# Optimization experiments

Measured on AMD Instinct MI355X. Metric: run time of the kernel, lower is better.

Reference implementation:

```python
import jax, jax.numpy as jnp
import numpy as np

N_LEVELS = 7  # log2(64) + 1

def setup_inputs() -> dict:
    key = jax.random.key(0)
    k1, k2, k3 = jax.random.split(key, 3)
    B, C, H, W = 32, 3, 64, 64
    flat_dim = C  # patch_size = 1
    n_embd = 896
    inner = n_embd // N_LEVELS  # 128
    return {
        "x": jax.random.normal(k1, (B, C, H, W), dtype=jnp.float32),
        "emb_w": jax.random.normal(k2, (flat_dim * N_LEVELS, n_embd), dtype=jnp.float32) * 0.05,
        "emb_b": jnp.zeros((n_embd,), dtype=jnp.float32),
        "cls_w": jax.random.normal(k3, (inner, 1000), dtype=jnp.float32) * 0.05,
        "cls_b": jnp.zeros((1000,), dtype=jnp.float32),
    }

def _token_tree(xp):
    # xp: (B, H, W, fd). For level l, every token gets the mean of its
    # aligned 2^l x 2^l block (quad-tree pooling), broadcast back to HxW.
    B, H, W, fd = xp.shape
    levels = []
    for l in range(N_LEVELS):
        bs = 2 ** l
        m = xp.reshape(B, H // bs, bs, W // bs, bs, fd).mean(axis=(2, 4))
        m = jnp.repeat(jnp.repeat(m, bs, axis=1), bs, axis=2)
        levels.append(m)
    return jnp.stack(levels, axis=3)  # (B, H, W, L, fd)

def reference(x, emb_w, emb_b, cls_w, cls_b):
    B, C, H, W = x.shape
    # patch extraction with patch_size=1 -> (B, H, W, C)
    xp = jnp.transpose(x, (0, 2, 3, 1))
    tree = _token_tree(xp)                      # (B,H,W,L,fd)
    flat = tree.reshape(B, H, W, -1)            # (B,H,W,L*fd)
    emb = flat @ emb_w + emb_b                  # (B,H,W,n_embd)
    inner = emb.shape[-1] // N_LEVELS
    emb = emb.reshape(B, H, W, N_LEVELS, inner)
    # num_layers = 0 -> nn.Sequential() is identity
    root = emb[:, :, :, N_LEVELS - 1, :]        # (B,H,W,inner)
    root_avg = root.mean(axis=(1, 2))           # (B,inner)
    return root_avg @ cls_w + cls_b             # (B,1000)
```

## Files before the change

kernel.cpp:

```cpp
#include <hip/hip_runtime.h>

#define BATCH   32
#define CHANS   3
#define HW      4096
#define NLEV    7
#define NEMBD   896
#define INNER   128
#define ROOTOFF 768
#define NCLS    1000


__global__ void k_reduce_x(const float* __restrict__ x, float* __restrict__ g) {
    const int bc = blockIdx.x;
    const float4* p4 = (const float4*)(x + (size_t)bc * HW);
    const int t = threadIdx.x;
    float s = 0.f;
#pragma unroll
    for (int i = 0; i < 4; ++i) {
        float4 v = p4[t + 256 * i];
        s += (v.x + v.y) + (v.z + v.w);
    }
#pragma unroll
    for (int off = 32; off > 0; off >>= 1)
        s += __shfl_down(s, off, 64);
    __shared__ float ls[4];
    if ((t & 63) == 0) ls[t >> 6] = s;
    __syncthreads();
    if (t == 0)
        g[bc] = (ls[0] + ls[1] + ls[2] + ls[3]) * (1.0f / HW);
}

__global__ __launch_bounds__(256) void k_head(
        const float* __restrict__ g,
        const float* __restrict__ emb_w,
        const float* __restrict__ emb_b,
        const float* __restrict__ cls_w,
        const float* __restrict__ cls_b,
        float* __restrict__ out) {
    const int t  = threadIdx.x;
    const int tx = t & 15;
    const int ty = t >> 4;
    const int k  = blockIdx.x * 16 + tx;
    const bool kok = (k < NCLS);

    __shared__ float wf0[INNER], wf1[INNER], wf2[INNER], eb[INNER];
    __shared__ float gsh[BATCH * CHANS];
    __shared__ float4 red[16][16];
    __shared__ float4 fin[16];

    if (t < INNER) {
        float a0 = 0.f, a1 = 0.f, a2 = 0.f;
#pragma unroll
        for (int l = 0; l < NLEV; ++l) {
            const float* row = emb_w + (size_t)(l * CHANS) * NEMBD + ROOTOFF + t;
            a0 += row[0 * NEMBD];
            a1 += row[1 * NEMBD];
            a2 += row[2 * NEMBD];
        }
        wf0[t] = a0; wf1[t] = a1; wf2[t] = a2;
        eb[t]  = emb_b[ROOTOFF + t];
    } else if (t < INNER + BATCH * CHANS) {
        gsh[t - INNER] = g[t - INNER];
    }
    __syncthreads();

    float m0 = 0.f, m1 = 0.f, m2 = 0.f, dd = 0.f;
    if (kok) {
        const int jb = ty * 8;
        float w[8];
#pragma unroll
        for (int jj = 0; jj < 8; ++jj)
            w[jj] = cls_w[(size_t)(jb + jj) * NCLS + k];
#pragma unroll
        for (int jj = 0; jj < 8; ++jj) {
            const int j = jb + jj;
            m0 += wf0[j] * w[jj];
            m1 += wf1[j] * w[jj];
            m2 += wf2[j] * w[jj];
            dd += eb[j]  * w[jj];
        }
    }
    red[ty][tx] = make_float4(m0, m1, m2, dd);
    __syncthreads();

    if (ty == 0) {
        float4 a = make_float4(0.f, 0.f, 0.f, kok ? cls_b[k] : 0.f);
#pragma unroll
        for (int yy = 0; yy < 16; ++yy) {
            float4 p = red[yy][tx];
            a.x += p.x; a.y += p.y; a.z += p.z; a.w += p.w;
        }
        fin[tx] = a;
    }
    __syncthreads();

    if (kok) {
        const float4 m = fin[tx];
#pragma unroll
        for (int h = 0; h < 2; ++h) {
            const int b = ty + 16 * h;
            const float* gb = gsh + b * CHANS;
            out[(size_t)b * NCLS + k] = m.w + gb[0] * m.x + gb[1] * m.y + gb[2] * m.z;
        }
    }
}

extern "C" void kernel_launch(void* const* d_in, const int* in_sizes, int n_in,
                              void* d_out, int out_size, void* d_ws, size_t ws_size,
                              hipStream_t stream) {
    const float* x     = (const float*)d_in[0];
    const float* emb_w = (const float*)d_in[1];
    const float* emb_b = (const float*)d_in[2];
    const float* cls_w = (const float*)d_in[3];
    const float* cls_b = (const float*)d_in[4];
    float* out = (float*)d_out;
    float* g   = (float*)d_ws;

    k_reduce_x<<<BATCH * CHANS, 256, 0, stream>>>(x, g);
    k_head<<<(NCLS + 15) / 16, 256, 0, stream>>>(g, emb_w, emb_b, cls_w, cls_b, out);
}
```

Baseline: 65.08 us.

## Fuse reduction and head kernels into one launch with atomic grid barrier

Merges the per-channel mean reduction and the classifier head into a single kernel of 96 blocks. Each block reduces its channel and publishes the mean through a global atomic counter, and the first 63 blocks do the head work, spinning on the counter before they read the means. This removes one kernel launch and the gap between the two kernels. In exchange it relies on all 96 blocks being co-resident and on an epoch-based counter that persists across launches.

```diff
diff --git a/kernel.cpp b/kernel.cpp
--- a/kernel.cpp
+++ b/kernel.cpp
@@ -8,43 +8,63 @@
 #define INNER   128
 #define ROOTOFF 768
 #define NCLS    1000
+#define NRED    (BATCH * CHANS)
+#define NHEAD   63
 
 
-__global__ void k_reduce_x(const float* __restrict__ x, float* __restrict__ g) {
-    const int bc = blockIdx.x;
-    const float4* p4 = (const float4*)(x + (size_t)bc * HW);
-    const int t = threadIdx.x;
-    float s = 0.f;
-#pragma unroll
-    for (int i = 0; i < 4; ++i) {
-        float4 v = p4[t + 256 * i];
-        s += (v.x + v.y) + (v.z + v.w);
-    }
-#pragma unroll
-    for (int off = 32; off > 0; off >>= 1)
-        s += __shfl_down(s, off, 64);
-    __shared__ float ls[4];
-    if ((t & 63) == 0) ls[t >> 6] = s;
-    __syncthreads();
-    if (t == 0)
-        g[bc] = (ls[0] + ls[1] + ls[2] + ls[3]) * (1.0f / HW);
-}
+__device__ unsigned g_done = 0;
+__device__ float    g_mean[NRED];
 
-__global__ __launch_bounds__(256) void k_head(
-        const float* __restrict__ g,
+__global__ __launch_bounds__(256) void k_fused(
+        const float* __restrict__ x,
         const float* __restrict__ emb_w,
         const float* __restrict__ emb_b,
         const float* __restrict__ cls_w,
         const float* __restrict__ cls_b,
         float* __restrict__ out) {
     const int t  = threadIdx.x;
+    const int bc = blockIdx.x;
+
+    unsigned target = 0;
+    if (t == 0) {
+        unsigned snap = __hip_atomic_load(&g_done, __ATOMIC_RELAXED,
+                                          __HIP_MEMORY_SCOPE_AGENT);
+        target = (snap / NRED) * NRED + NRED;
+    }
+
+    __shared__ float ls[4];
+
+    {
+        const float4* p4 = (const float4*)(x + (size_t)bc * HW);
+        float s = 0.f;
+#pragma unroll
+        for (int i = 0; i < 4; ++i) {
+            float4 v = p4[t + 256 * i];
+            s += (v.x + v.y) + (v.z + v.w);
+        }
+#pragma unroll
+        for (int off = 32; off > 0; off >>= 1)
+            s += __shfl_down(s, off, 64);
+        if ((t & 63) == 0) ls[t >> 6] = s;
+        __syncthreads();
+        if (t == 0) {
+            float mean = (ls[0] + ls[1] + ls[2] + ls[3]) * (1.0f / HW);
+            __hip_atomic_store(&g_mean[bc], mean, __ATOMIC_RELAXED,
+                               __HIP_MEMORY_SCOPE_AGENT);
+            __hip_atomic_fetch_add(&g_done, 1u, __ATOMIC_RELEASE,
+                                   __HIP_MEMORY_SCOPE_AGENT);
+        }
+    }
+
+    if (bc >= NHEAD) return;
+
     const int tx = t & 15;
     const int ty = t >> 4;
-    const int k  = blockIdx.x * 16 + tx;
+    const int k  = bc * 16 + tx;
     const bool kok = (k < NCLS);
 
     __shared__ float wf0[INNER], wf1[INNER], wf2[INNER], eb[INNER];
-    __shared__ float gsh[BATCH * CHANS];
+    __shared__ float gsh[NRED];
     __shared__ float4 red[16][16];
     __shared__ float4 fin[16];
 
@@ -59,8 +79,6 @@
         }
         wf0[t] = a0; wf1[t] = a1; wf2[t] = a2;
         eb[t]  = emb_b[ROOTOFF + t];
-    } else if (t < INNER + BATCH * CHANS) {
-        gsh[t - INNER] = g[t - INNER];
     }
     __syncthreads();
 
@@ -92,6 +110,17 @@
         }
         fin[tx] = a;
     }
+
+    if (t == 0) {
+        while ((int)(__hip_atomic_load(&g_done, __ATOMIC_ACQUIRE,
+                                       __HIP_MEMORY_SCOPE_AGENT) - target) < 0)
+            __builtin_amdgcn_s_sleep(1);
+    }
+    __syncthreads();
+
+    if (t < NRED)
+        gsh[t] = __hip_atomic_load(&g_mean[t], __ATOMIC_RELAXED,
+                                   __HIP_MEMORY_SCOPE_AGENT);
     __syncthreads();
 
     if (kok) {
@@ -114,8 +143,7 @@
     const float* cls_w = (const float*)d_in[3];
     const float* cls_b = (const float*)d_in[4];
     float* out = (float*)d_out;
-    float* g   = (float*)d_ws;
+    (void)d_ws; (void)ws_size;
 
-    k_reduce_x<<<BATCH * CHANS, 256, 0, stream>>>(x, g);
-    k_head<<<(NCLS + 15) / 16, 256, 0, stream>>>(g, emb_w, emb_b, cls_w, cls_b, out);
+    k_fused<<<NRED, 256, 0, stream>>>(x, emb_w, emb_b, cls_w, cls_b, out);
 }
```

Result: no change. 64.34 us (-1.1%).
